# Optimization experiments

Hardware: AMD Instinct MI355X
Metric: run time of the kernel (lower is better)

The kernel has to match this reference:

```python
import jax, jax.numpy as jnp
import numpy as np

N, E, IN_D, H, OUT_D = 50000, 800000, 128, 64, 64


def setup_inputs() -> dict:
    key = jax.random.key(0)
    ks = jax.random.split(key, 16)
    s = lambda k, shape: jax.random.normal(k, shape, dtype=jnp.float32) * (1.0 / np.sqrt(shape[0]))
    return {
        "x": jax.random.normal(ks[0], (N, IN_D), dtype=jnp.float32),
        "edge_index": jax.random.randint(ks[1], (2, E), 0, N, dtype=jnp.int32),
        "W1": s(ks[2], (IN_D, H)), "b1": jnp.zeros((H,), jnp.float32),
        "W2": s(ks[3], (H, 2 * H)), "b2": jnp.zeros((2 * H,), jnp.float32),
        "W3": s(ks[4], (2 * H, 4 * H)), "b3": jnp.zeros((4 * H,), jnp.float32),
        "dec1_w": s(ks[5], (4 * H, 2 * H, 2)), "dec1_b": jnp.zeros((2 * H,), jnp.float32),
        "dec2_w": s(ks[6], (2 * H, H, 2)), "dec2_b": jnp.zeros((H,), jnp.float32),
        "dec3_w": s(ks[7], (H, H, 2)), "dec3_b": jnp.zeros((H,), jnp.float32),
        "skip1_w": s(ks[8], (2 * H, 2 * H)), "skip1_b": jnp.zeros((2 * H,), jnp.float32),
        "skip2_w": s(ks[9], (H, H)), "skip2_b": jnp.zeros((H,), jnp.float32),
        "fin_w": s(ks[10], (OUT_D, 8 * H)), "fin_b": jnp.zeros((OUT_D,), jnp.float32),
    }


def _deconv2(x, w, b):
    # ConvTranspose1d(kernel=2, stride=2): [n,c,l] x [c,o,2] -> [n,o,2l]
    y = jnp.einsum('ncl,cok->nolk', x, w)
    n, o = x.shape[0], w.shape[1]
    return y.reshape(n, o, -1) + b[None, :, None]


def reference(x, edge_index, W1, b1, W2, b2, W3, b3, dec1_w, dec1_b, dec2_w, dec2_b,
              dec3_w, dec3_b, skip1_w, skip1_b, skip2_w, skip2_b, fin_w, fin_b):
    n = x.shape[0]
    loop = jnp.arange(n, dtype=edge_index.dtype)
    src = jnp.concatenate([edge_index[0], loop])
    tgt = jnp.concatenate([edge_index[1], loop])
    deg = jax.ops.segment_sum(jnp.ones_like(src, dtype=x.dtype), tgt, num_segments=n)
    dinv = jax.lax.rsqrt(deg)  # deg >= 1 due to self-loops
    norm = dinv[src] * dinv[tgt]  # [E+N]

    def gcn(h, W, b):
        hw = h @ W
        agg = jax.ops.segment_sum(hw[src] * norm[:, None], tgt, num_segments=n)
        return agg + b

    x1 = jax.nn.gelu(gcn(x, W1, b1))    # [N, H]
    x2 = jax.nn.gelu(gcn(x1, W2, b2))   # [N, 2H]
    x3 = jax.nn.gelu(gcn(x2, W3, b3))   # [N, 4H]

    d = _deconv2(x3[:, :, None], dec1_w, dec1_b)           # [N, 2H, 2]
    d = d + (x2 @ skip1_w.T + skip1_b)[:, :, None]
    d = _deconv2(d, dec2_w, dec2_b)                        # [N, H, 4]
    d = d + (x1 @ skip2_w.T + skip2_b)[:, :, None]
    d = _deconv2(d, dec3_w, dec3_b)                        # [N, H, 8]
    out = d.reshape(n, -1) @ fin_w.T + fin_b               # [N, OUT_D]
    return out
```

## Files before the change

kernel.cpp:

```cpp
#include <hip/hip_runtime.h>
#include <hip/hip_bf16.h>

typedef __attribute__((ext_vector_type(8))) short short8_t;
typedef __attribute__((ext_vector_type(4))) float f32x4;

#define CAP 64

__device__ __forceinline__ float gelu_f(float x) {
    float x3 = x * x * x;
    return 0.5f * x * (1.0f + tanhf(0.7978845608028654f * (x + 0.044715f * x3)));
}
__device__ __forceinline__ float b2f(unsigned short u) {
    union { float f; unsigned int i; } c; c.i = ((unsigned int)u) << 16; return c.f;
}
__device__ __forceinline__ unsigned short f2bu(float f) {
    union { float f; unsigned int i; } c; c.f = f;
    unsigned int r = c.i + 0x7fffu + ((c.i >> 16) & 1u);
    return (unsigned short)(r >> 16);
}


__device__ __forceinline__ void d_EF(int bid, int t, const float* __restrict__ dec3_w,
                                     const float* __restrict__ fin_w, float* __restrict__ EF) {
    int i2 = bid * 4 + (t >> 6), od = t & 63;
    int c3 = i2 >> 2, pp = i2 & 3;
    const float* d3 = dec3_w + c3 * 128;
    const float* fw = fin_w + od * 512;
    float s = 0.f;
    #pragma unroll
    for (int o3 = 0; o3 < 64; ++o3) {
        s += d3[o3 * 2 + 0] * fw[o3 * 8 + pp * 2 + 0];
        s += d3[o3 * 2 + 1] * fw[o3 * 8 + pp * 2 + 1];
    }
    EF[i2 * 64 + od] = s;
}

__device__ __forceinline__ void d_CEF(int bid, int t, const float* __restrict__ dec2_w,
                                      const float* __restrict__ EF, float* __restrict__ CEF) {
    int i1 = bid * 4 + (t >> 6), od = t & 63;
    int c2 = i1 >> 1, lp = i1 & 1;
    const float* d2 = dec2_w + c2 * 128;
    float s = 0.f;
    #pragma unroll
    for (int o2 = 0; o2 < 64; ++o2) {
        s += d2[o2 * 2 + 0] * EF[(o2 * 4 + lp * 2 + 0) * 64 + od];
        s += d2[o2 * 2 + 1] * EF[(o2 * 4 + lp * 2 + 1) * 64 + od];
    }
    CEF[i1 * 64 + od] = s;
}

__device__ __forceinline__ void d_comp(int sb, int od,
                       const float* __restrict__ dec1_w, const float* __restrict__ skip1_w,
                       const float* __restrict__ skip2_w,
                       const float* __restrict__ dec1_b, const float* __restrict__ skip1_b,
                       const float* __restrict__ dec2_b, const float* __restrict__ skip2_b,
                       const float* __restrict__ dec3_b, const float* __restrict__ fin_w,
                       const float* __restrict__ fin_b,
                       const float* __restrict__ CEF, const float* __restrict__ EF,
                       unsigned short* __restrict__ McatT, float* __restrict__ m0) {
    if (sb < 256) {
        const float* d1 = dec1_w + sb * 256;
        float s = 0.f;
        for (int j = 0; j < 256; ++j) s += d1[j] * CEF[j * 64 + od];
        McatT[od * 448 + sb] = f2bu(s);
    } else if (sb < 384) {
        int c = sb - 256;
        float s = 0.f;
        for (int j = 0; j < 256; ++j) s += skip1_w[(j >> 1) * 128 + c] * CEF[j * 64 + od];
        McatT[od * 448 + sb] = f2bu(s);
    } else if (sb < 448) {
        int c = sb - 384;
        float s = 0.f;
        for (int j = 0; j < 256; ++j) s += skip2_w[(j >> 2) * 64 + c] * EF[j * 64 + od];
        McatT[od * 448 + sb] = f2bu(s);
    } else {
        float s = fin_b[od];
        for (int j = 0; j < 256; ++j) s += (dec1_b[j >> 1] + skip1_b[j >> 1]) * CEF[j * 64 + od];
        for (int j = 0; j < 256; ++j) s += (dec2_b[j >> 2] + skip2_b[j >> 2]) * EF[j * 64 + od];
        for (int j = 0; j < 512; ++j) s += dec3_b[j >> 3] * fin_w[od * 512 + j];
        m0[od] = s;
    }
}

__device__ __forceinline__ void d_wconv(int bid, int t,
                        const float* __restrict__ W1, const float* __restrict__ W2,
                        const float* __restrict__ W3,
                        unsigned short* __restrict__ W1T, unsigned short* __restrict__ W2T,
                        unsigned short* __restrict__ W3T) {
    int i = bid * 256 + t;
    if (i < 8192) {
        int k = i >> 6, n = i & 63;
        W1T[n * 128 + k] = f2bu(W1[i]);
    } else if (i < 16384) {
        int j = i - 8192; int k = j >> 7, n = j & 127;
        W2T[n * 64 + k] = f2bu(W2[j]);
    } else if (i < 49152) {
        int j = i - 16384; int k = j >> 8, n = j & 255;
        W3T[n * 128 + k] = f2bu(W3[j]);
    }
}

__device__ __forceinline__ void d_fillx(int bid, int t, const int* __restrict__ src,
                                        const int* __restrict__ tgt, int E,
                                        int* __restrict__ cnt, int* __restrict__ csr) {
    int i = (bid * 256 + t) * 8;
    if (i + 7 < E) {
        int4 t0 = *(const int4*)(tgt + i);
        int4 t1 = *(const int4*)(tgt + i + 4);
        int4 s0 = *(const int4*)(src + i);
        int4 s1 = *(const int4*)(src + i + 4);
        int k0 = atomicAdd(&cnt[t0.x], 1);
        int k1 = atomicAdd(&cnt[t0.y], 1);
        int k2 = atomicAdd(&cnt[t0.z], 1);
        int k3 = atomicAdd(&cnt[t0.w], 1);
        int k4 = atomicAdd(&cnt[t1.x], 1);
        int k5 = atomicAdd(&cnt[t1.y], 1);
        int k6 = atomicAdd(&cnt[t1.z], 1);
        int k7 = atomicAdd(&cnt[t1.w], 1);
        if (k0 < CAP) csr[(t0.x << 6) + k0] = s0.x;
        if (k1 < CAP) csr[(t0.y << 6) + k1] = s0.y;
        if (k2 < CAP) csr[(t0.z << 6) + k2] = s0.z;
        if (k3 < CAP) csr[(t0.w << 6) + k3] = s0.w;
        if (k4 < CAP) csr[(t1.x << 6) + k4] = s1.x;
        if (k5 < CAP) csr[(t1.y << 6) + k5] = s1.y;
        if (k6 < CAP) csr[(t1.z << 6) + k6] = s1.z;
        if (k7 < CAP) csr[(t1.w << 6) + k7] = s1.w;
    } else {
        for (int k = i; k < E; ++k) {
            int tt = tgt[k];
            int kk = atomicAdd(&cnt[tt], 1);
            if (kk < CAP) csr[(tt << 6) + kk] = src[k];
        }
    }
}

template<bool A32, bool BIAS, bool GELU, bool OUT32>
__device__ __forceinline__ void d_gmm(
    int bx, int by,
    const unsigned short* __restrict__ A, const float* __restrict__ Af, int lda,
    const unsigned short* __restrict__ Bt,
    const float* __restrict__ bias,
    void* __restrict__ Cv, int ldc, int M, int K) {
    constexpr int LDS_R = 72;
    __shared__ unsigned short As[64 * LDS_R];
    __shared__ unsigned short Bs[64 * LDS_R];
    const int tid = threadIdx.x;
    const int r0 = bx * 64, c0 = by * 64;
    const int w = tid >> 6, lane = tid & 63;
    const int wm = (w >> 1) * 32, wn = (w & 1) * 32;
    const int fr = lane & 15, kg = lane >> 4;
    f32x4 acc[2][2];
    #pragma unroll
    for (int m = 0; m < 2; ++m)
        #pragma unroll
        for (int n = 0; n < 2; ++n) { f32x4 z = {0.f, 0.f, 0.f, 0.f}; acc[m][n] = z; }

    const int sr = tid >> 2, sc = (tid & 3) * 16;
    const bool aok = (r0 + sr) < M;
    const unsigned short* ag = A32 ? nullptr : (A + (size_t)(r0 + sr) * lda + sc);
    const float* agf = A32 ? (Af + (size_t)(r0 + sr) * lda + sc) : nullptr;
    const unsigned short* bg = Bt + (size_t)(c0 + sr) * K + sc;

    for (int kt = 0; kt < K; kt += 64) {
        if (aok) {
            if constexpr (A32) {
                float4 f0 = *(const float4*)(agf + kt);
                float4 f1 = *(const float4*)(agf + kt + 4);
                float4 f2 = *(const float4*)(agf + kt + 8);
                float4 f3 = *(const float4*)(agf + kt + 12);
                unsigned short o[16] = { f2bu(f0.x), f2bu(f0.y), f2bu(f0.z), f2bu(f0.w),
                                         f2bu(f1.x), f2bu(f1.y), f2bu(f1.z), f2bu(f1.w),
                                         f2bu(f2.x), f2bu(f2.y), f2bu(f2.z), f2bu(f2.w),
                                         f2bu(f3.x), f2bu(f3.y), f2bu(f3.z), f2bu(f3.w) };
                *(uint4*)&As[sr * LDS_R + sc]     = ((const uint4*)o)[0];
                *(uint4*)&As[sr * LDS_R + sc + 8] = ((const uint4*)o)[1];
            } else {
                *(uint4*)&As[sr * LDS_R + sc]     = *(const uint4*)(ag + kt);
                *(uint4*)&As[sr * LDS_R + sc + 8] = *(const uint4*)(ag + kt + 8);
            }
        }
        *(uint4*)&Bs[sr * LDS_R + sc]     = *(const uint4*)(bg + kt);
        *(uint4*)&Bs[sr * LDS_R + sc + 8] = *(const uint4*)(bg + kt + 8);
        __syncthreads();
        #pragma unroll
        for (int s2 = 0; s2 < 2; ++s2) {
            short8_t afr[2], bfr[2];
            #pragma unroll
            for (int n = 0; n < 2; ++n)
                bfr[n] = *(const short8_t*)&Bs[(wn + n * 16 + fr) * LDS_R + s2 * 32 + kg * 8];
            #pragma unroll
            for (int m = 0; m < 2; ++m)
                afr[m] = *(const short8_t*)&As[(wm + m * 16 + fr) * LDS_R + s2 * 32 + kg * 8];
            #pragma unroll
            for (int m = 0; m < 2; ++m)
                #pragma unroll
                for (int n = 0; n < 2; ++n)
                    acc[m][n] = __builtin_amdgcn_mfma_f32_16x16x32_bf16(afr[m], bfr[n], acc[m][n], 0, 0, 0);
        }
        __syncthreads();
    }
    #pragma unroll
    for (int m = 0; m < 2; ++m) {
        #pragma unroll
        for (int n = 0; n < 2; ++n) {
            #pragma unroll
            for (int j = 0; j < 4; ++j) {
                int row = r0 + wm + m * 16 + kg * 4 + j;
                int col = c0 + wn + n * 16 + fr;
                if (row < M) {
                    float xv = acc[m][n][j];
                    if (BIAS) xv += bias[col];
                    if (GELU) xv = gelu_f(xv);
                    if (OUT32) ((float*)Cv)[(size_t)row * ldc + col] = xv;
                    else ((unsigned short*)Cv)[(size_t)row * ldc + col] = f2bu(xv);
                }
            }
        }
    }
}

template<int F, int LPN, bool EPI>
__device__ __forceinline__ void d_aggb(
    int bid,
    const unsigned short* __restrict__ g, int ldi,
    const int* __restrict__ cnt, const int* __restrict__ csr,
    const float* __restrict__ bias,
    unsigned short* __restrict__ out, int ldo, int N) {
    constexpr int SLOTS = 64 / LPN;
    static_assert(F / LPN == 8, "V must be 8");
    __shared__ int   sIdx[4][2][CAP];
    __shared__ float sW[4][2][CAP];
    int tid = threadIdx.x;
    int lane = tid & 63, wv = tid >> 6;
    int v0 = bid * 8 + wv * 2;
    int v1 = v0 + 1;
    bool ok0 = v0 < N, ok1 = v1 < N;
    int vc0 = ok0 ? v0 : 0, vc1 = ok1 ? v1 : 0;
    int slot = lane / LPN, fl = lane % LPN;
    int fo = fl * 8;
    int deg0 = cnt[vc0], deg1 = cnt[vc1];
    float dv0 = rsqrtf((float)(deg0 + 1)), dv1 = rsqrtf((float)(deg1 + 1));
    int degc0 = min(deg0, CAP - 1), degc1 = min(deg1, CAP - 1);
    int ua = (lane < degc0) ? csr[(vc0 << 6) + lane] : vc0;
    int ub = (lane < degc1) ? csr[(vc1 << 6) + lane] : vc1;
    int ca = cnt[ua], cb = cnt[ub];
    float wa = (lane < degc0) ? rsqrtf((float)(ca + 1)) * dv0
                              : ((lane == degc0) ? dv0 * dv0 : 0.f);
    float wb = (lane < degc1) ? rsqrtf((float)(cb + 1)) * dv1
                              : ((lane == degc1) ? dv1 * dv1 : 0.f);
    sIdx[wv][0][lane] = ua;  sW[wv][0][lane] = wa;
    sIdx[wv][1][lane] = ub;  sW[wv][1][lane] = wb;
    __syncthreads();
    int cntE0 = ok0 ? degc0 + 1 : 0;
    int cntE1 = ok1 ? degc1 + 1 : 0;
    int cmax = max(cntE0, cntE1);
    float acc0[8] = {}, acc1[8] = {};
    const unsigned short* hbase = g + fo;
    int j = slot;
    for (; j + SLOTS < cmax; j += 2 * SLOTS) {
        int u00 = sIdx[wv][0][j];          float w00 = sW[wv][0][j];
        int u01 = sIdx[wv][0][j + SLOTS];  float w01 = sW[wv][0][j + SLOTS];
        int u10 = sIdx[wv][1][j];          float w10 = sW[wv][1][j];
        int u11 = sIdx[wv][1][j + SLOTS];  float w11 = sW[wv][1][j + SLOTS];
        uint4 t00 = *(const uint4*)(hbase + (size_t)u00 * ldi);
        uint4 t01 = *(const uint4*)(hbase + (size_t)u01 * ldi);
        uint4 t10 = *(const uint4*)(hbase + (size_t)u10 * ldi);
        uint4 t11 = *(const uint4*)(hbase + (size_t)u11 * ldi);
        const unsigned short* p00 = (const unsigned short*)&t00;
        const unsigned short* p01 = (const unsigned short*)&t01;
        const unsigned short* p10 = (const unsigned short*)&t10;
        const unsigned short* p11 = (const unsigned short*)&t11;
        #pragma unroll
        for (int q = 0; q < 8; ++q) {
            acc0[q] = fmaf(b2f(p00[q]), w00, acc0[q]);
            acc1[q] = fmaf(b2f(p10[q]), w10, acc1[q]);
        }
        #pragma unroll
        for (int q = 0; q < 8; ++q) {
            acc0[q] = fmaf(b2f(p01[q]), w01, acc0[q]);
            acc1[q] = fmaf(b2f(p11[q]), w11, acc1[q]);
        }
    }
    if (j < cmax) {
        int u0 = sIdx[wv][0][j];  float w0 = sW[wv][0][j];
        int u1 = sIdx[wv][1][j];  float w1 = sW[wv][1][j];
        uint4 t0 = *(const uint4*)(hbase + (size_t)u0 * ldi);
        uint4 t1 = *(const uint4*)(hbase + (size_t)u1 * ldi);
        const unsigned short* p0 = (const unsigned short*)&t0;
        const unsigned short* p1 = (const unsigned short*)&t1;
        #pragma unroll
        for (int q = 0; q < 8; ++q) {
            acc0[q] = fmaf(b2f(p0[q]), w0, acc0[q]);
            acc1[q] = fmaf(b2f(p1[q]), w1, acc1[q]);
        }
    }
    #pragma unroll
    for (int off = LPN; off < 64; off <<= 1)
        #pragma unroll
        for (int q = 0; q < 8; ++q) {
            acc0[q] += __shfl_xor(acc0[q], off, 64);
            acc1[q] += __shfl_xor(acc1[q], off, 64);
        }
    if (slot == 0) {
        unsigned short o0[8], o1[8];
        #pragma unroll
        for (int q = 0; q < 8; ++q) {
            float x0 = acc0[q], x1 = acc1[q];
            if (EPI) {
                float bq = bias[fo + q];
                x0 = gelu_f(x0 + bq);
                x1 = gelu_f(x1 + bq);
            }
            o0[q] = f2bu(x0);
            o1[q] = f2bu(x1);
        }
        if (ok0) *(uint4*)(out + (size_t)v0 * ldo + fo) = *(const uint4*)o0;
        if (ok1) *(uint4*)(out + (size_t)v1 * ldo + fo) = *(const uint4*)o1;
    }
}


template<bool A32, bool BIAS, bool GELU, bool OUT32>
__global__ __launch_bounds__(256) void k_gmm(
    const unsigned short* __restrict__ A, const float* __restrict__ Af, int lda,
    const unsigned short* __restrict__ Bt,
    const float* __restrict__ bias,
    void* __restrict__ Cv, int ldc, int M, int K) {
    d_gmm<A32, BIAS, GELU, OUT32>(blockIdx.x, blockIdx.y, A, Af, lda, Bt, bias, Cv, ldc, M, K);
}

template<int F, int LPN, bool EPI>
__global__ __launch_bounds__(256) void k_aggb(
    const unsigned short* __restrict__ g, int ldi,
    const int* __restrict__ cnt, const int* __restrict__ csr,
    const float* __restrict__ bias,
    unsigned short* __restrict__ out, int ldo, int N) {
    d_aggb<F, LPN, EPI>(blockIdx.x, g, ldi, cnt, csr, bias, out, ldo, N);
}

__global__ __launch_bounds__(256) void k_mega0(
    const float* __restrict__ W1, const float* __restrict__ W2, const float* __restrict__ W3,
    unsigned short* __restrict__ W1T, unsigned short* __restrict__ W2T,
    unsigned short* __restrict__ W3T,
    const float* __restrict__ dec3_w, const float* __restrict__ fin_w, float* __restrict__ EF,
    int* __restrict__ cnt, int N) {
    int b = blockIdx.x, t = threadIdx.x;
    if (b < 192) d_wconv(b, t, W1, W2, W3, W1T, W2T, W3T);
    else if (b < 256) d_EF(b - 192, t, dec3_w, fin_w, EF);
    else { int i = (b - 256) * 256 + t; if (i < N) cnt[i] = 0; }
}

__global__ __launch_bounds__(256) void k_megaA(
    const int* __restrict__ src, const int* __restrict__ tgt, int E,
    int* __restrict__ cnt, int* __restrict__ csr, int nf,
    const float* __restrict__ x, const unsigned short* __restrict__ W1T,
    unsigned short* __restrict__ hw1, int M, int ng,
    const float* __restrict__ dec2_w, const float* __restrict__ EF, float* __restrict__ CEF) {
    int b = blockIdx.x;
    if (b < nf)
        d_fillx(b, threadIdx.x, src, tgt, E, cnt, csr);
    else if (b < nf + ng)
        d_gmm<true, false, false, false>(b - nf, 0, nullptr, x, 128, W1T,
                                         (const float*)nullptr, hw1, 64, M, 128);
    else
        d_CEF(b - nf - ng, threadIdx.x, dec2_w, EF, CEF);
}

__global__ __launch_bounds__(256) void k_megaB(
    const unsigned short* __restrict__ hw1,
    const int* __restrict__ cnt, const int* __restrict__ csr,
    const float* __restrict__ b1, unsigned short* __restrict__ x1out, int N, int na,
    const float* __restrict__ dec1_w, const float* __restrict__ skip1_w,
    const float* __restrict__ skip2_w,
    const float* __restrict__ dec1_b, const float* __restrict__ skip1_b,
    const float* __restrict__ dec2_b, const float* __restrict__ skip2_b,
    const float* __restrict__ dec3_b, const float* __restrict__ fin_w,
    const float* __restrict__ fin_b,
    const float* __restrict__ CEF, const float* __restrict__ EF,
    unsigned short* __restrict__ McatT, float* __restrict__ m0) {
    int b = blockIdx.x, t = threadIdx.x;
    if (b < na) {
        d_aggb<64, 8, true>(b, hw1, 64, cnt, csr, b1, x1out, 448, N);
    } else {
        int sb = (b - na) * 4 + (t >> 6);
        if (sb <= 448)
            d_comp(sb, t & 63, dec1_w, skip1_w, skip2_w, dec1_b, skip1_b, dec2_b, skip2_b,
                   dec3_b, fin_w, fin_b, CEF, EF, McatT, m0);
    }
}

extern "C" void kernel_launch(void* const* d_in, const int* in_sizes, int n_in,
                              void* d_out, int out_size, void* d_ws, size_t ws_size,
                              hipStream_t stream) {
    const float* x       = (const float*)d_in[0];
    const int*   ei      = (const int*)d_in[1];
    const float* W1      = (const float*)d_in[2];
    const float* b1      = (const float*)d_in[3];
    const float* W2      = (const float*)d_in[4];
    const float* b2      = (const float*)d_in[5];
    const float* W3      = (const float*)d_in[6];
    const float* b3      = (const float*)d_in[7];
    const float* dec1_w  = (const float*)d_in[8];
    const float* dec1_b  = (const float*)d_in[9];
    const float* dec2_w  = (const float*)d_in[10];
    const float* dec2_b  = (const float*)d_in[11];
    const float* dec3_w  = (const float*)d_in[12];
    const float* dec3_b  = (const float*)d_in[13];
    const float* skip1_w = (const float*)d_in[14];
    const float* skip1_b = (const float*)d_in[15];
    const float* skip2_w = (const float*)d_in[16];
    const float* skip2_b = (const float*)d_in[17];
    const float* fin_w   = (const float*)d_in[18];
    const float* fin_b   = (const float*)d_in[19];

    const int N = in_sizes[0] / 128;
    const int E = in_sizes[1] / 2;
    const int* e_src = ei;
    const int* e_tgt = ei + E;

    char* p = (char*)d_ws;
    auto alloc = [&](size_t bytes) -> void* {
        void* r = p;
        p += (bytes + 255) & ~(size_t)255;
        return r;
    };
    int*   cnt     = (int*)alloc((size_t)N * 4);
    int*   csr     = (int*)alloc((size_t)N * CAP * 4);
    float* EF      = (float*)alloc(256 * 64 * 4);
    float* CEF     = (float*)alloc(256 * 64 * 4);
    float* m0      = (float*)alloc(64 * 4);
    unsigned short* McatT = (unsigned short*)alloc(64 * 448 * 2);
    unsigned short* W1T   = (unsigned short*)alloc(64 * 128 * 2);
    unsigned short* W2T   = (unsigned short*)alloc(128 * 64 * 2);
    unsigned short* W3T   = (unsigned short*)alloc(256 * 128 * 2);
    unsigned short* hw1   = (unsigned short*)alloc((size_t)N * 64 * 2);
    unsigned short* a1    = (unsigned short*)alloc((size_t)N * 64 * 2);
    unsigned short* xcat  = (unsigned short*)alloc((size_t)N * 448 * 2);
    unsigned short* a2    = hw1;
    if ((size_t)(p - (char*)d_ws) > ws_size) return;

    const int nf = (E / 8 + 255) / 256;
    const int mg = (N + 63) / 64;
    const int ag = (N + 7) / 8;
    const int compb = (449 + 3) / 4;
    const int zb = (N + 255) / 256;

    k_mega0<<<dim3(192 + 64 + zb), dim3(256), 0, stream>>>(
        W1, W2, W3, W1T, W2T, W3T, dec3_w, fin_w, EF, cnt, N);

    k_megaA<<<dim3(nf + mg + 64), dim3(256), 0, stream>>>(
        e_src, e_tgt, E, cnt, csr, nf, x, W1T, hw1, N, mg, dec2_w, EF, CEF);

    k_megaB<<<dim3(ag + compb), dim3(256), 0, stream>>>(
        hw1, cnt, csr, b1, xcat + 384, N, ag,
        dec1_w, skip1_w, skip2_w, dec1_b, skip1_b, dec2_b, skip2_b, dec3_b,
        fin_w, fin_b, CEF, EF, McatT, m0);

    k_aggb<64, 8, false><<<dim3(ag), dim3(256), 0, stream>>>(
        xcat + 384, 448, cnt, csr, (const float*)nullptr, a1, 64, N);
    k_gmm<false, true, true, false><<<dim3(mg, 2), dim3(256), 0, stream>>>(
        a1, nullptr, 64, W2T, b2, xcat + 256, 448, N, 64);

    k_aggb<128, 16, false><<<dim3(ag), dim3(256), 0, stream>>>(
        xcat + 256, 448, cnt, csr, (const float*)nullptr, a2, 128, N);
    k_gmm<false, true, true, false><<<dim3(mg, 4), dim3(256), 0, stream>>>(
        a2, nullptr, 128, W3T, b3, xcat, 448, N, 128);

    k_gmm<false, true, false, true><<<dim3(mg, 1), dim3(256), 0, stream>>>(
        xcat, nullptr, 448, McatT, m0, d_out, 64, N, 448);
}
```

Baseline: 203.3 us.

## Split final projection into per-layer partial GEMMs fused with aggregation launches

Replaces the single final GEMM over the concatenated [x3|x2|x1] buffer (K=448) with three partial GEMMs that accumulate into the fp32 output. The x1 and x2 partials run as extra blocks inside the same launches as the next aggregation, so that work overlaps with the gather-bound aggregation. The concat buffer is split into separate compact x1/x2/x3 arrays, giving the aggregation kernels denser strides. In exchange the output is read and written three times with read-modify-write, and more workspace is used.

```diff
diff --git a/kernel.cpp b/kernel.cpp
--- a/kernel.cpp
+++ b/kernel.cpp
@@ -134,11 +134,11 @@
     }
 }
 
-template<bool A32, bool BIAS, bool GELU, bool OUT32>
+template<bool A32, bool BIAS, bool GELU, bool OUT32, bool ACC>
 __device__ __forceinline__ void d_gmm(
     int bx, int by,
     const unsigned short* __restrict__ A, const float* __restrict__ Af, int lda,
-    const unsigned short* __restrict__ Bt,
+    const unsigned short* __restrict__ Bt, int ldb,
     const float* __restrict__ bias,
     void* __restrict__ Cv, int ldc, int M, int K) {
     constexpr int LDS_R = 72;
@@ -159,7 +159,7 @@
     const bool aok = (r0 + sr) < M;
     const unsigned short* ag = A32 ? nullptr : (A + (size_t)(r0 + sr) * lda + sc);
     const float* agf = A32 ? (Af + (size_t)(r0 + sr) * lda + sc) : nullptr;
-    const unsigned short* bg = Bt + (size_t)(c0 + sr) * K + sc;
+    const unsigned short* bg = Bt + (size_t)(c0 + sr) * ldb + sc;
 
     for (int kt = 0; kt < K; kt += 64) {
         if (aok) {
@@ -211,8 +211,13 @@
                     float xv = acc[m][n][j];
                     if (BIAS) xv += bias[col];
                     if (GELU) xv = gelu_f(xv);
-                    if (OUT32) ((float*)Cv)[(size_t)row * ldc + col] = xv;
-                    else ((unsigned short*)Cv)[(size_t)row * ldc + col] = f2bu(xv);
+                    if (OUT32) {
+                        float* cp = (float*)Cv + (size_t)row * ldc + col;
+                        if (ACC) xv += *cp;
+                        *cp = xv;
+                    } else {
+                        ((unsigned short*)Cv)[(size_t)row * ldc + col] = f2bu(xv);
+                    }
                 }
             }
         }
@@ -320,22 +325,14 @@
 }
 
 
-template<bool A32, bool BIAS, bool GELU, bool OUT32>
+template<bool A32, bool BIAS, bool GELU, bool OUT32, bool ACC>
 __global__ __launch_bounds__(256) void k_gmm(
     const unsigned short* __restrict__ A, const float* __restrict__ Af, int lda,
-    const unsigned short* __restrict__ Bt,
+    const unsigned short* __restrict__ Bt, int ldb,
     const float* __restrict__ bias,
     void* __restrict__ Cv, int ldc, int M, int K) {
-    d_gmm<A32, BIAS, GELU, OUT32>(blockIdx.x, blockIdx.y, A, Af, lda, Bt, bias, Cv, ldc, M, K);
-}
-
-template<int F, int LPN, bool EPI>
-__global__ __launch_bounds__(256) void k_aggb(
-    const unsigned short* __restrict__ g, int ldi,
-    const int* __restrict__ cnt, const int* __restrict__ csr,
-    const float* __restrict__ bias,
-    unsigned short* __restrict__ out, int ldo, int N) {
-    d_aggb<F, LPN, EPI>(blockIdx.x, g, ldi, cnt, csr, bias, out, ldo, N);
+    d_gmm<A32, BIAS, GELU, OUT32, ACC>(blockIdx.x, blockIdx.y, A, Af, lda, Bt, ldb, bias,
+                                       Cv, ldc, M, K);
 }
 
 __global__ __launch_bounds__(256) void k_mega0(
@@ -360,8 +357,8 @@
     if (b < nf)
         d_fillx(b, threadIdx.x, src, tgt, E, cnt, csr);
     else if (b < nf + ng)
-        d_gmm<true, false, false, false>(b - nf, 0, nullptr, x, 128, W1T,
-                                         (const float*)nullptr, hw1, 64, M, 128);
+        d_gmm<true, false, false, false, false>(b - nf, 0, nullptr, x, 128, W1T, 128,
+                                                (const float*)nullptr, hw1, 64, M, 128);
     else
         d_CEF(b - nf - ng, threadIdx.x, dec2_w, EF, CEF);
 }
@@ -369,7 +366,7 @@
 __global__ __launch_bounds__(256) void k_megaB(
     const unsigned short* __restrict__ hw1,
     const int* __restrict__ cnt, const int* __restrict__ csr,
-    const float* __restrict__ b1, unsigned short* __restrict__ x1out, int N, int na,
+    const float* __restrict__ b1, unsigned short* __restrict__ x1, int N, int na,
     const float* __restrict__ dec1_w, const float* __restrict__ skip1_w,
     const float* __restrict__ skip2_w,
     const float* __restrict__ dec1_b, const float* __restrict__ skip1_b,
@@ -380,13 +377,39 @@
     unsigned short* __restrict__ McatT, float* __restrict__ m0) {
     int b = blockIdx.x, t = threadIdx.x;
     if (b < na) {
-        d_aggb<64, 8, true>(b, hw1, 64, cnt, csr, b1, x1out, 448, N);
+        d_aggb<64, 8, true>(b, hw1, 64, cnt, csr, b1, x1, 64, N);
     } else {
         int sb = (b - na) * 4 + (t >> 6);
         if (sb <= 448)
             d_comp(sb, t & 63, dec1_w, skip1_w, skip2_w, dec1_b, skip1_b, dec2_b, skip2_b,
                    dec3_b, fin_w, fin_b, CEF, EF, McatT, m0);
     }
+}
+
+__global__ __launch_bounds__(256) void k_megaC(
+    const unsigned short* __restrict__ x1, const unsigned short* __restrict__ McatT,
+    const float* __restrict__ m0, float* __restrict__ dout, int N, int ng,
+    const int* __restrict__ cnt, const int* __restrict__ csr,
+    unsigned short* __restrict__ a1) {
+    int b = blockIdx.x;
+    if (b < ng)
+        d_gmm<false, true, false, true, false>(b, 0, x1, nullptr, 64, McatT + 384, 448,
+                                               m0, dout, 64, N, 64);
+    else
+        d_aggb<64, 8, false>(b - ng, x1, 64, cnt, csr, (const float*)nullptr, a1, 64, N);
+}
+
+__global__ __launch_bounds__(256) void k_megaE(
+    const unsigned short* __restrict__ x2, const unsigned short* __restrict__ McatT,
+    float* __restrict__ dout, int N, int ng,
+    const int* __restrict__ cnt, const int* __restrict__ csr,
+    unsigned short* __restrict__ a2) {
+    int b = blockIdx.x;
+    if (b < ng)
+        d_gmm<false, false, false, true, true>(b, 0, x2, nullptr, 128, McatT + 256, 448,
+                                               (const float*)nullptr, dout, 64, N, 128);
+    else
+        d_aggb<128, 16, false>(b - ng, x2, 128, cnt, csr, (const float*)nullptr, a2, 128, N);
 }
 
 extern "C" void kernel_launch(void* const* d_in, const int* in_sizes, int n_in,
@@ -434,9 +457,11 @@
     unsigned short* W2T   = (unsigned short*)alloc(128 * 64 * 2);
     unsigned short* W3T   = (unsigned short*)alloc(256 * 128 * 2);
     unsigned short* hw1   = (unsigned short*)alloc((size_t)N * 64 * 2);
+    unsigned short* x1    = (unsigned short*)alloc((size_t)N * 64 * 2);
     unsigned short* a1    = (unsigned short*)alloc((size_t)N * 64 * 2);
-    unsigned short* xcat  = (unsigned short*)alloc((size_t)N * 448 * 2);
-    unsigned short* a2    = hw1;
+    unsigned short* x2    = (unsigned short*)alloc((size_t)N * 128 * 2);
+    unsigned short* a2    = (unsigned short*)alloc((size_t)N * 128 * 2);
+    unsigned short* x3    = (unsigned short*)alloc((size_t)N * 256 * 2);
     if ((size_t)(p - (char*)d_ws) > ws_size) return;
 
     const int nf = (E / 8 + 255) / 256;
@@ -452,20 +477,22 @@
         e_src, e_tgt, E, cnt, csr, nf, x, W1T, hw1, N, mg, dec2_w, EF, CEF);
 
     k_megaB<<<dim3(ag + compb), dim3(256), 0, stream>>>(
-        hw1, cnt, csr, b1, xcat + 384, N, ag,
+        hw1, cnt, csr, b1, x1, N, ag,
         dec1_w, skip1_w, skip2_w, dec1_b, skip1_b, dec2_b, skip2_b, dec3_b,
         fin_w, fin_b, CEF, EF, McatT, m0);
 
-    k_aggb<64, 8, false><<<dim3(ag), dim3(256), 0, stream>>>(
-        xcat + 384, 448, cnt, csr, (const float*)nullptr, a1, 64, N);
-    k_gmm<false, true, true, false><<<dim3(mg, 2), dim3(256), 0, stream>>>(
-        a1, nullptr, 64, W2T, b2, xcat + 256, 448, N, 64);
-
-    k_aggb<128, 16, false><<<dim3(ag), dim3(256), 0, stream>>>(
-        xcat + 256, 448, cnt, csr, (const float*)nullptr, a2, 128, N);
-    k_gmm<false, true, true, false><<<dim3(mg, 4), dim3(256), 0, stream>>>(
-        a2, nullptr, 128, W3T, b3, xcat, 448, N, 128);
-
-    k_gmm<false, true, false, true><<<dim3(mg, 1), dim3(256), 0, stream>>>(
-        xcat, nullptr, 448, McatT, m0, d_out, 64, N, 448);
-}
+    k_megaC<<<dim3(mg + ag), dim3(256), 0, stream>>>(
+        x1, McatT, m0, (float*)d_out, N, mg, cnt, csr, a1);
+
+    k_gmm<false, true, true, false, false><<<dim3(mg, 2), dim3(256), 0, stream>>>(
+        a1, nullptr, 64, W2T, 64, b2, x2, 128, N, 64);
+
+    k_megaE<<<dim3(mg + ag), dim3(256), 0, stream>>>(
+        x2, McatT, (float*)d_out, N, mg, cnt, csr, a2);
+
+    k_gmm<false, true, true, false, false><<<dim3(mg, 4), dim3(256), 0, stream>>>(
+        a2, nullptr, 128, W3T, 128, b3, x3, 256, N, 128);
+
+    k_gmm<false, false, false, true, true><<<dim3(mg, 1), dim3(256), 0, stream>>>(
+        x3, nullptr, 256, McatT, 448, (const float*)nullptr, (float*)d_out, 64, N, 256);
+}
```

Result: slower. 215.6 us (+6.1%).
